# Kernel tuning notes

Hardware: AMD Instinct MI355X
Metric: run time of the kernel (lower is better)

The kernel has to match this reference:

```python
import jax, jax.numpy as jnp
import numpy as np

# Dims. NOTE: TransmorpherLayer2d passes (dim_head, num_heads) positionally into an
# attention class whose signature is (num_heads, dim_head) -> attention runs with
# H = dim_head = 64 heads of size Dh = num_heads = 12. embed_dim D = 768 either way.
B, S, L = 1, 64, 512
H, Dh = 64, 12
D = H * Dh          # 768
DFF = 3072
EPS = 1e-5


def _ln(x, g, b):
    m = x.mean(-1, keepdims=True)
    v = ((x - m) ** 2).mean(-1, keepdims=True)
    return (x - m) / jnp.sqrt(v + EPS) * g + b


def setup_inputs() -> dict:
    key = jax.random.key(0)
    ks = jax.random.split(key, 6)
    sd = 0.02
    p = {
        'x': jax.random.normal(ks[0], (B, S, L, D), jnp.float32),
        'w_row': jax.random.normal(ks[1], (D, 3 * D), jnp.float32) * sd,
        'b_row': jnp.zeros((3 * D,), jnp.float32),
        'w_col': jax.random.normal(ks[2], (D, 3 * D), jnp.float32) * sd,
        'b_col': jnp.zeros((3 * D,), jnp.float32),
        'g_a1': jnp.ones((D,), jnp.float32), 'be_a1': jnp.zeros((D,), jnp.float32),
        'g_a2': jnp.ones((D,), jnp.float32), 'be_a2': jnp.zeros((D,), jnp.float32),
        'w1': jax.random.normal(ks[3], (D, DFF), jnp.float32) * sd,
        'b1f': jnp.zeros((DFF,), jnp.float32),
        'w2': jax.random.normal(ks[4], (DFF, D), jnp.float32) * sd,
        'b2f': jnp.zeros((D,), jnp.float32),
        'g_n1': jnp.ones((D,), jnp.float32), 'be_n1': jnp.zeros((D,), jnp.float32),
        'g_n2': jnp.ones((D,), jnp.float32), 'be_n2': jnp.zeros((D,), jnp.float32),
    }
    return p


def reference(x, w_row, b_row, w_col, b_col, g_a1, be_a1, g_a2, be_a2,
              w1, b1f, w2, b2f, g_n1, be_n1, g_n2, be_n2):
    def qkv(t, w, b):
        q, k, v = jnp.split(t @ w + b, 3, axis=-1)
        rs = lambda a: a.reshape(B, S, L, H, Dh)
        return rs(q), rs(k), rs(v)

    # ---- TiedAxialSelfAttention2d (no 1/sqrt(d) scaling, tied over S) ----
    q, k, v = qkv(x, w_row, b_row)
    row_attn = jax.nn.softmax(jnp.einsum('bsihc,bsjhc->bhij', q, k), axis=-1)  # [B,H,L,L]
    row_out = jnp.einsum('bhij,bsjhd->bsihd', row_attn, v).reshape(B, S, L, D)
    out = _ln(x + row_out, g_a1, be_a1)

    q, k, v = qkv(out, w_col, b_col)
    col_attn = jax.nn.softmax(jnp.einsum('bilhc,bjlhc->bhijl', q, k), axis=-2)  # [B,H,S,S,L]
    col_out = jnp.einsum('bhijl,bjlhd->bilhd', col_attn, v).reshape(B, S, L, D)
    out = _ln(out + col_out, g_a2, be_a2)

    # ---- TransmorpherLayer2d residual + FFN (post-LN) ----
    y = _ln(x + out, g_n1, be_n1)
    ff = jax.nn.relu(y @ w1 + b1f) @ w2 + b2f
    return _ln(y + ff, g_n2, be_n2)
```

## Files before the change

kernel.cpp:

```cpp
#include <hip/hip_runtime.h>

typedef unsigned short u16;
typedef unsigned int u32;
typedef __attribute__((ext_vector_type(8))) short short8;
typedef __attribute__((ext_vector_type(4))) float floatx4;

#define LN_EPS 1e-5f
#define REG 6291456L

__device__ __forceinline__ float b2f(u16 u) {
    return __builtin_bit_cast(float, (u32)u << 16);
}
__device__ __forceinline__ u16 f2b(float f) {
    u32 x = __builtin_bit_cast(u32, f);
    return (u16)((x + 0x7fffu + ((x >> 16) & 1u)) >> 16);
}

__device__ __forceinline__ void ld12f(const float* p, float* d) {
    float4 a = ((const float4*)p)[0];
    float4 b = ((const float4*)p)[1];
    float4 c = ((const float4*)p)[2];
    d[0]=a.x; d[1]=a.y; d[2]=a.z;  d[3]=a.w;
    d[4]=b.x; d[5]=b.y; d[6]=b.z;  d[7]=b.w;
    d[8]=c.x; d[9]=c.y; d[10]=c.z; d[11]=c.w;
}
__device__ __forceinline__ void ld12b(const u16* p, float* d) {
    uint2 a = ((const uint2*)p)[0];
    uint2 b = ((const uint2*)p)[1];
    uint2 c = ((const uint2*)p)[2];
    d[0]=b2f((u16)a.x); d[1]=b2f((u16)(a.x>>16)); d[2]=b2f((u16)a.y);  d[3]=b2f((u16)(a.y>>16));
    d[4]=b2f((u16)b.x); d[5]=b2f((u16)(b.x>>16)); d[6]=b2f((u16)b.y);  d[7]=b2f((u16)(b.y>>16));
    d[8]=b2f((u16)c.x); d[9]=b2f((u16)(c.x>>16)); d[10]=b2f((u16)c.y); d[11]=b2f((u16)(c.y>>16));
}
__device__ __forceinline__ void st12f(float* p, const float* d) {
    ((float4*)p)[0] = make_float4(d[0], d[1], d[2], d[3]);
    ((float4*)p)[1] = make_float4(d[4], d[5], d[6], d[7]);
    ((float4*)p)[2] = make_float4(d[8], d[9], d[10], d[11]);
}
__device__ __forceinline__ void st12b(u16* p, const float* d) {
    uint2 a, b, c;
    a.x = (u32)f2b(d[0])  | ((u32)f2b(d[1])  << 16);
    a.y = (u32)f2b(d[2])  | ((u32)f2b(d[3])  << 16);
    b.x = (u32)f2b(d[4])  | ((u32)f2b(d[5])  << 16);
    b.y = (u32)f2b(d[6])  | ((u32)f2b(d[7])  << 16);
    c.x = (u32)f2b(d[8])  | ((u32)f2b(d[9])  << 16);
    c.y = (u32)f2b(d[10]) | ((u32)f2b(d[11]) << 16);
    ((uint2*)p)[0] = a; ((uint2*)p)[1] = b; ((uint2*)p)[2] = c;
}
__device__ __forceinline__ void wred2(float& a, float& b) {
#pragma unroll
    for (int o = 32; o > 0; o >>= 1) {
        a += __shfl_xor(a, o, 64);
        b += __shfl_xor(b, o, 64);
    }
}

__device__ __forceinline__ void gload16(const u16* g, u16* l) {
    __builtin_amdgcn_global_load_lds(
        (const __attribute__((address_space(1))) void*)g,
        (__attribute__((address_space(3))) void*)l, 16, 0, 0);
}

template<int N> __device__ __forceinline__ void wait_vm() {
    if constexpr (N == 0)      asm volatile("s_waitcnt vmcnt(0)" ::: "memory");
    else if constexpr (N == 4) asm volatile("s_waitcnt vmcnt(4)" ::: "memory");
    else if constexpr (N == 5) asm volatile("s_waitcnt vmcnt(5)" ::: "memory");
    else                       asm volatile("s_waitcnt vmcnt(0)" ::: "memory");
}

template<int BN_, int EPI, int RELU, int HASBIAS, int SMAJ>
__global__ __launch_bounds__(256, 2) void gemm_dma(
    const u16* __restrict__ A, const u16* __restrict__ BT,
    const float* __restrict__ bias, void* __restrict__ C,
    int Nb, int K, long sA, long sB, long sC, int colbase)
{
    constexpr int NCH  = (128 + BN_) / 64;
    constexpr int JF   = BN_ / 32;
    constexpr int TILE = (128 + BN_) * 32;
    __shared__ u16 lds[3 * TILE];

    const u16* Az = A + (long)blockIdx.z * sA;
    const u16* Bz = BT + (long)blockIdx.z * sB;
    const int n0 = blockIdx.x * BN_;
    const int tid = threadIdx.x;
    const int lane = tid & 63;
    const int wm = ((tid >> 6) >> 1) * 64;
    const int wn = ((tid >> 6) & 1) * (BN_ / 2);
    const int lrow = lane & 15;
    const int quad = lane >> 4;

    floatx4 acc[4][JF];
#pragma unroll
    for (int i = 0; i < 4; i++)
#pragma unroll
        for (int j = 0; j < JF; j++)
            acc[i][j] = (floatx4){0.f, 0.f, 0.f, 0.f};

    const u16* sbase[NCH];
    int doff[NCH];
#pragma unroll
    for (int it = 0; it < NCH; it++) {
        const int idx = tid + it * 256;
        const int slot = idx & 3;
        doff[it] = idx * 8;
        if (idx < 512) {
            const int row = idx >> 2;
            const int ch  = (slot ^ ((row >> 1) & 3)) * 8;
            const long grow = SMAJ
                ? ((long)(row >> 1) * 512 + (blockIdx.y << 1) + (row & 1))
                : ((long)blockIdx.y * 128 + row);
            sbase[it] = Az + grow * K + ch;
        } else {
            const int row = (idx - 512) >> 2;
            const int ch  = (slot ^ ((row >> 1) & 3)) * 8;
            sbase[it] = Bz + (long)(n0 + row) * K + ch;
        }
    }

    int aoff[4], boff[JF];
#pragma unroll
    for (int i = 0; i < 4; i++) {
        const int r = wm + i * 16 + lrow;
        aoff[i] = r * 32 + ((quad ^ ((r >> 1) & 3)) * 8);
    }
#pragma unroll
    for (int j = 0; j < JF; j++) {
        const int r = wn + j * 16 + lrow;
        boff[j] = 4096 + r * 32 + ((quad ^ ((r >> 1) & 3)) * 8);
    }

#pragma unroll
    for (int it = 0; it < NCH; it++)
        gload16(sbase[it], &lds[doff[it]]);
    if (K > 32) {
#pragma unroll
        for (int it = 0; it < NCH; it++)
            gload16(sbase[it] + 32, &lds[TILE + doff[it]]);
    }
    __builtin_amdgcn_sched_barrier(0);

    int bufc = 0;
    for (int kt = 0; kt < K; kt += 32) {
        if (kt + 32 >= K) wait_vm<0>();
        else              wait_vm<NCH>();
        __builtin_amdgcn_s_barrier();
        __builtin_amdgcn_sched_barrier(0);

        if (kt + 64 < K) {
            int nb = bufc + 2; if (nb >= 3) nb -= 3;
            const int nbo = nb * TILE;
#pragma unroll
            for (int it = 0; it < NCH; it++)
                gload16(sbase[it] + kt + 64, &lds[nbo + doff[it]]);
        }
        __builtin_amdgcn_sched_barrier(0);

        const int b0 = bufc * TILE;
        short8 af[4], bfr[JF];
#pragma unroll
        for (int i = 0; i < 4; i++)
            af[i] = *(const short8*)&lds[b0 + aoff[i]];
#pragma unroll
        for (int j = 0; j < JF; j++)
            bfr[j] = *(const short8*)&lds[b0 + boff[j]];
#pragma unroll
        for (int i = 0; i < 4; i++)
#pragma unroll
            for (int j = 0; j < JF; j++)
                acc[i][j] = __builtin_amdgcn_mfma_f32_16x16x32_bf16(
                    af[i], bfr[j], acc[i][j], 0, 0, 0);

        __builtin_amdgcn_sched_barrier(0);
        if (++bufc == 3) bufc = 0;
    }

    const int z = blockIdx.z;
#pragma unroll
    for (int j = 0; j < JF; j++) {
        const int n = n0 + wn + j * 16 + lrow;
        int t = 0, jj = n;
        if (EPI == 8 || EPI == 9) { t = n / 192; jj = n - t * 192; }
        const int hl = jj / 12;
        const int cc = jj - hl * 12;
        float bv = 0.f;
        if (HASBIAS)
            bv = (EPI == 8 || EPI == 9) ? bias[t * 768 + colbase + jj]
                                        : bias[colbase + n];
#pragma unroll
        for (int i = 0; i < 4; i++) {
            const int mb = wm + i * 16 + quad * 4;
#pragma unroll
            for (int r = 0; r < 4; r++) {
                const int ml = mb + r;
                float v = acc[i][j][r] + bv;
                if (RELU) v = fmaxf(v, 0.f);
                if (EPI == 0) {
                    const long m = (long)blockIdx.y * 128 + ml;
                    ((u16*)C)[m * Nb + n] = f2b(v);
                } else if (EPI == 1) {
                    const long m = (long)blockIdx.y * 128 + ml;
                    ((float*)C)[(long)z * sC + m * Nb + n] = v;
                } else if (EPI == 3) {
                    const int gm = blockIdx.y * 128 + ml;
                    const int s = gm >> 9, iL = gm & 511;
                    ((u16*)C)[(long)hl * 393216 + (long)(s * 12 + cc) * 512 + iL] = f2b(v);
                } else if (EPI == 4) {
                    const int m = blockIdx.y * 128 + ml;
                    ((u16*)C)[((long)hl * 512 + m) * 768 + colbase + z * 12 + cc] = f2b(v);
                } else if (EPI == 8) {
                    const int s = ml >> 1, iL = (blockIdx.y << 1) + (ml & 1);
                    ((u16*)C)[(long)t * REG + ((long)hl * 512 + iL) * 768 + s * 12 + cc] = f2b(v);
                } else if (EPI == 9) {
                    const int s = ml >> 1, l = (blockIdx.y << 1) + (ml & 1);
                    ((u16*)C)[(long)t * REG + (long)hl * 393216 + (long)l * 768 + s * 12 + cc] = f2b(v);
                }
            }
        }
    }
}

__global__ __launch_bounds__(256) void cast_kernel(
    const float* __restrict__ X, u16* __restrict__ Xb)
{
    const long i = ((long)blockIdx.x * 256 + threadIdx.x) * 8;
    float4 a = *(const float4*)(X + i);
    float4 b = *(const float4*)(X + i + 4);
    u16 t8[8] = { f2b(a.x), f2b(a.y), f2b(a.z), f2b(a.w),
                  f2b(b.x), f2b(b.y), f2b(b.z), f2b(b.w) };
    *(uint4*)(Xb + i) = *(const uint4*)t8;
}

__global__ __launch_bounds__(256) void transpose_kernel(
    const float* __restrict__ In, u16* __restrict__ Out, int R, int Ccols)
{
    __shared__ u16 tile[32][33];
    int tx = threadIdx.x & 31;
    int ty = threadIdx.x >> 5;
    int c0 = blockIdx.x * 32;
    int r0 = blockIdx.y * 32;
#pragma unroll
    for (int rr = 0; rr < 32; rr += 8)
        tile[ty + rr][tx] = f2b(In[(long)(r0 + ty + rr) * Ccols + c0 + tx]);
    __syncthreads();
#pragma unroll
    for (int rr = 0; rr < 32; rr += 8)
        Out[(long)(c0 + ty + rr) * R + r0 + tx] = tile[tx][ty + rr];
}

__global__ __launch_bounds__(256) void pack_qk_kernel(
    const float* __restrict__ In, u16* __restrict__ Out)
{
    __shared__ u16 tile[32][33];
    int tx = threadIdx.x & 31;
    int ty = threadIdx.x >> 5;
    int p0 = blockIdx.x * 32;
    int k0 = blockIdx.y * 32;
    int hg = p0 / 384, rem = p0 % 384;
    int t = rem / 192, j0 = rem % 192;
    int c0 = t * 768 + hg * 192 + j0;
#pragma unroll
    for (int rr = 0; rr < 32; rr += 8)
        tile[ty + rr][tx] = f2b(In[(long)(k0 + ty + rr) * 2304 + c0 + tx]);
    __syncthreads();
#pragma unroll
    for (int rr = 0; rr < 32; rr += 8)
        Out[(long)(p0 + ty + rr) * 768 + k0 + tx] = tile[tx][ty + rr];
}

__global__ __launch_bounds__(256) void pack_v_kernel(
    const float* __restrict__ In, u16* __restrict__ Out)
{
    __shared__ u16 tile[32][33];
    int tx = threadIdx.x & 31;
    int ty = threadIdx.x >> 5;
    int p0 = blockIdx.x * 32;
    int k0 = blockIdx.y * 32;
    int hg = p0 / 192, j0 = p0 % 192;
    int c0 = 1536 + hg * 192 + j0;
#pragma unroll
    for (int rr = 0; rr < 32; rr += 8)
        tile[ty + rr][tx] = f2b(In[(long)(k0 + ty + rr) * 2304 + c0 + tx]);
    __syncthreads();
#pragma unroll
    for (int rr = 0; rr < 32; rr += 8)
        Out[(long)(p0 + ty + rr) * 768 + k0 + tx] = tile[tx][ty + rr];
}

__global__ __launch_bounds__(256) void qkv_pack_kernel(
    const float* __restrict__ In, u16* __restrict__ Out)
{
    __shared__ u16 tile[32][33];
    int tx = threadIdx.x & 31;
    int ty = threadIdx.x >> 5;
    int p0 = blockIdx.x * 32;
    int k0 = blockIdx.y * 32;
    int hg = p0 / 576, r0 = p0 % 576;
    int t = r0 / 192, j0 = r0 % 192;
    int c0 = t * 768 + hg * 192 + j0;
#pragma unroll
    for (int rr = 0; rr < 32; rr += 8)
        tile[ty + rr][tx] = f2b(In[(long)(k0 + ty + rr) * 2304 + c0 + tx]);
    __syncthreads();
#pragma unroll
    for (int rr = 0; rr < 32; rr += 8)
        Out[(long)(p0 + ty + rr) * 768 + k0 + tx] = tile[tx][ty + rr];
}

__global__ __launch_bounds__(256) void softmax_kernel(
    const float* __restrict__ S, u16* __restrict__ P)
{
    const long r = (long)blockIdx.x * 4 + (threadIdx.x >> 6);
    const int lane = threadIdx.x & 63;
    const float* sp = S + r * 512 + lane * 8;
    float4 a = ((const float4*)sp)[0];
    float4 b = ((const float4*)sp)[1];
    float v[8] = {a.x, a.y, a.z, a.w, b.x, b.y, b.z, b.w};
    float mx = v[0];
#pragma unroll
    for (int e = 1; e < 8; e++) mx = fmaxf(mx, v[e]);
#pragma unroll
    for (int o = 32; o > 0; o >>= 1) mx = fmaxf(mx, __shfl_xor(mx, o, 64));
    float sum = 0.f;
#pragma unroll
    for (int e = 0; e < 8; e++) { v[e] = __expf(v[e] - mx); sum += v[e]; }
#pragma unroll
    for (int o = 32; o > 0; o >>= 1) sum += __shfl_xor(sum, o, 64);
    float inv = 1.0f / sum;
    uint4 o4;
    o4.x = (u32)f2b(v[0] * inv) | ((u32)f2b(v[1] * inv) << 16);
    o4.y = (u32)f2b(v[2] * inv) | ((u32)f2b(v[3] * inv) << 16);
    o4.z = (u32)f2b(v[4] * inv) | ((u32)f2b(v[5] * inv) << 16);
    o4.w = (u32)f2b(v[6] * inv) | ((u32)f2b(v[7] * inv) << 16);
    *(uint4*)(P + r * 512 + lane * 8) = o4;
}

template<int AF, int BF, int OF>
__global__ __launch_bounds__(256) void ln_add_kernel(
    const void* __restrict__ Xa, const void* __restrict__ Xb,
    const float* __restrict__ g, const float* __restrict__ be,
    void* __restrict__ Out)
{
    const long r = (long)blockIdx.x * 4 + (threadIdx.x >> 6);
    const int lane = threadIdx.x & 63;
    const long c0 = r * 768 + lane * 12;
    float va[12], vb[12], v[12];
    if (AF) ld12f((const float*)Xa + c0, va);
    else    ld12b((const u16*)Xa + c0, va);
    if (BF) ld12f((const float*)Xb + c0, vb);
    else    ld12b((const u16*)Xb + c0, vb);
    float sm = 0.f, s2 = 0.f;
#pragma unroll
    for (int e = 0; e < 12; e++) {
        v[e] = va[e] + vb[e];
        sm += v[e]; s2 += v[e] * v[e];
    }
    wred2(sm, s2);
    float mean = sm * (1.0f / 768.0f);
    float var  = s2 * (1.0f / 768.0f) - mean * mean;
    float rstd = rsqrtf(var + LN_EPS);
    float gv[12], bv[12], o[12];
    ld12f(g + lane * 12, gv);
    ld12f(be + lane * 12, bv);
#pragma unroll
    for (int e = 0; e < 12; e++)
        o[e] = (v[e] - mean) * rstd * gv[e] + bv[e];
    if (OF) st12f((float*)Out + c0, o);
    else    st12b((u16*)Out + c0, o);
}

__global__ __launch_bounds__(256) void ln_ln_kernel(
    const u16* __restrict__ A, const u16* __restrict__ B,
    const float* __restrict__ X,
    const float* __restrict__ g1, const float* __restrict__ be1,
    const float* __restrict__ g2, const float* __restrict__ be2,
    float* __restrict__ Out, u16* __restrict__ Outb)
{
    const long r = (long)blockIdx.x * 4 + (threadIdx.x >> 6);
    const int lane = threadIdx.x & 63;
    const long c0 = r * 768 + lane * 12;
    float ua[12], ub[12], u[12];
    ld12b(A + c0, ua);
    ld12b(B + c0, ub);
    float sm = 0.f, s2 = 0.f;
#pragma unroll
    for (int e = 0; e < 12; e++) {
        u[e] = ua[e] + ub[e];
        sm += u[e]; s2 += u[e] * u[e];
    }
    wred2(sm, s2);
    float mean1 = sm * (1.0f / 768.0f);
    float var1  = s2 * (1.0f / 768.0f) - mean1 * mean1;
    float rstd1 = rsqrtf(var1 + LN_EPS);

    float xx[12], g1v[12], b1v[12], w[12];
    ld12f(X + c0, xx);
    ld12f(g1 + lane * 12, g1v);
    ld12f(be1 + lane * 12, b1v);
    sm = 0.f; s2 = 0.f;
#pragma unroll
    for (int e = 0; e < 12; e++) {
        float tv = (u[e] - mean1) * rstd1 * g1v[e] + b1v[e];
        w[e] = xx[e] + tv;
        sm += w[e]; s2 += w[e] * w[e];
    }
    wred2(sm, s2);
    float mean2 = sm * (1.0f / 768.0f);
    float var2  = s2 * (1.0f / 768.0f) - mean2 * mean2;
    float rstd2 = rsqrtf(var2 + LN_EPS);

    float g2v[12], b2v[12], o[12];
    ld12f(g2 + lane * 12, g2v);
    ld12f(be2 + lane * 12, b2v);
#pragma unroll
    for (int e = 0; e < 12; e++)
        o[e] = (w[e] - mean2) * rstd2 * g2v[e] + b2v[e];
    st12f(Out + c0, o);
    st12b(Outb + c0, o);
}

__global__ __launch_bounds__(64) void col_attn_kernel(
    const u16* __restrict__ qc, const u16* __restrict__ kc,
    const u16* __restrict__ vc, u16* __restrict__ Out, int hbase)
{
    const int hh = blockIdx.x >> 9;
    const int l  = blockIdx.x & 511;
    const int i  = threadIdx.x;
    const long base = ((long)hh * 512 + l) * 768 + (long)i * 12;
    __shared__ float Ks[64][12];
    __shared__ float Vs[64][12];
    float q[12], kk[12], vv[12];
    ld12b(qc + base, q);
    ld12b(kc + base, kk);
    ld12b(vc + base, vv);
#pragma unroll
    for (int c = 0; c < 12; c++) { Ks[i][c] = kk[c]; Vs[i][c] = vv[c]; }
    __syncthreads();
    float sc[64];
#pragma unroll
    for (int j = 0; j < 64; j++) {
        float a = 0.f;
#pragma unroll
        for (int c = 0; c < 12; c++) a += q[c] * Ks[j][c];
        sc[j] = a;
    }
    float m = sc[0];
#pragma unroll
    for (int j = 1; j < 64; j++) m = fmaxf(m, sc[j]);
    float sum = 0.f;
#pragma unroll
    for (int j = 0; j < 64; j++) { sc[j] = __expf(sc[j] - m); sum += sc[j]; }
    float inv = 1.0f / sum;
    float o[12];
#pragma unroll
    for (int c = 0; c < 12; c++) o[c] = 0.f;
#pragma unroll
    for (int j = 0; j < 64; j++) {
        float p = sc[j] * inv;
#pragma unroll
        for (int c = 0; c < 12; c++) o[c] += p * Vs[j][c];
    }
    u16* op = Out + ((long)i * 512 + l) * 768 + hbase + hh * 12;
    st12b(op, o);
}

extern "C" void kernel_launch(void* const* d_in, const int* in_sizes, int n_in,
                              void* d_out, int out_size, void* d_ws, size_t ws_size,
                              hipStream_t stream)
{
    (void)in_sizes; (void)n_in; (void)out_size; (void)ws_size;

    const float* x     = (const float*)d_in[0];
    const float* w_row = (const float*)d_in[1];
    const float* b_row = (const float*)d_in[2];
    const float* w_col = (const float*)d_in[3];
    const float* b_col = (const float*)d_in[4];
    const float* g_a1  = (const float*)d_in[5];
    const float* be_a1 = (const float*)d_in[6];
    const float* g_a2  = (const float*)d_in[7];
    const float* be_a2 = (const float*)d_in[8];
    const float* w1    = (const float*)d_in[9];
    const float* b1f   = (const float*)d_in[10];
    const float* w2    = (const float*)d_in[11];
    const float* b2f_  = (const float*)d_in[12];
    const float* g_n1  = (const float*)d_in[13];
    const float* be_n1 = (const float*)d_in[14];
    const float* g_n2  = (const float*)d_in[15];
    const float* be_n2 = (const float*)d_in[16];
    float* outp = (float*)d_out;

    char* wp = (char*)d_ws;
    auto alloc = [&](size_t bytes) -> void* {
        void* p = (void*)wp;
        wp += (bytes + 255) & ~(size_t)255;
        return p;
    };
    u16*   wPqk   = (u16*)alloc((size_t)1536 * 768 * 2);
    u16*   wPv    = (u16*)alloc((size_t)768 * 768 * 2);
    u16*   wPcol  = (u16*)alloc((size_t)2304 * 768 * 2);
    u16*   w1T    = (u16*)alloc((size_t)3072 * 768 * 2);
    u16*   w2T    = (u16*)alloc((size_t)768 * 3072 * 2);
    u16*   bufA   = (u16*)alloc((size_t)32768 * 768 * 2);
    u16*   bufB   = (u16*)alloc((size_t)32768 * 768 * 2);
    u16*   qkvg   = (u16*)alloc((size_t)3 * 16 * 512 * 768 * 2);
    float* scores = (float*)alloc((size_t)16 * 512 * 512 * 4);
    u16*   probs  = (u16*)alloc((size_t)16 * 512 * 512 * 2);
    u16*   hidden = qkvg;
    u16*   xb     = bufB;
    u16*   ybf    = bufB;
    float* y      = outp;

    pack_qk_kernel<<<dim3(48, 24), 256, 0, stream>>>(w_row, wPqk);
    pack_v_kernel<<<dim3(24, 24), 256, 0, stream>>>(w_row, wPv);
    qkv_pack_kernel<<<dim3(72, 24), 256, 0, stream>>>(w_col, wPcol);
    transpose_kernel<<<dim3(96, 24), 256, 0, stream>>>(w1, w1T, 768, 3072);
    transpose_kernel<<<dim3(24, 96), 256, 0, stream>>>(w2, w2T, 3072, 768);
    cast_kernel<<<12288, 256, 0, stream>>>(x, xb);

    for (int hg = 0; hg < 4; hg++) {
        gemm_dma<192, 8, 0, 1, 1><<<dim3(2, 256), 256, 0, stream>>>(
            xb, wPqk + (long)hg * 384 * 768, b_row, qkvg,
            384, 768, 0, 0, 0, hg * 192);
        gemm_dma<192, 3, 0, 1, 0><<<dim3(1, 256), 256, 0, stream>>>(
            xb, wPv + (long)hg * 192 * 768, b_row, qkvg + 2 * REG,
            192, 768, 0, 0, 0, 1536 + hg * 192);
        gemm_dma<128, 1, 0, 0, 0><<<dim3(4, 4, 16), 256, 0, stream>>>(
            qkvg, qkvg + REG, nullptr, scores,
            512, 768, (long)512 * 768, (long)512 * 768, (long)512 * 512, 0);
        softmax_kernel<<<2048, 256, 0, stream>>>(scores, probs);
        gemm_dma<128, 4, 0, 0, 0><<<dim3(6, 4, 16), 256, 0, stream>>>(
            probs, qkvg + 2 * REG, nullptr, bufA,
            768, 512, (long)512 * 512, (long)768 * 512, 0, hg * 192);
    }
    ln_add_kernel<1, 0, 0><<<8192, 256, 0, stream>>>(x, bufA, g_a1, be_a1, bufB);

    for (int hg = 0; hg < 4; hg++) {
        gemm_dma<192, 9, 0, 1, 1><<<dim3(3, 256), 256, 0, stream>>>(
            bufB, wPcol + (long)hg * 576 * 768, b_col, qkvg,
            576, 768, 0, 0, 0, hg * 192);
        col_attn_kernel<<<8192, 64, 0, stream>>>(
            qkvg, qkvg + REG, qkvg + 2 * REG, bufA, hg * 192);
    }
    ln_ln_kernel<<<8192, 256, 0, stream>>>(
        bufB, bufA, x, g_a2, be_a2, g_n1, be_n1, y, ybf);

    for (int mc = 0; mc < 4; mc++) {
        const long off = (long)mc * 8192 * 768;
        gemm_dma<192, 0, 1, 1, 0><<<dim3(16, 64), 256, 0, stream>>>(
            ybf + off, w1T, b1f, hidden, 3072, 768, 0, 0, 0, 0);
        gemm_dma<192, 0, 0, 1, 0><<<dim3(4, 64), 256, 0, stream>>>(
            hidden, w2T, b2f_, bufA + off, 768, 3072, 0, 0, 0, 0);
    }
    ln_add_kernel<1, 0, 1><<<8192, 256, 0, stream>>>(y, bufA, g_n2, be_n2, outp);
}
```

Measured before the change: 1.580 ms.

## Process all attention heads in one pass when workspace allows, halve FFN chunks

When the workspace is large enough, the row and column attention stages run over all 64 heads in a single set of launches instead of four head-group loops. The QKV epilogues gain a head-group index and a runtime stride to support this, and probs reuses bufB. The FFN is split into two row chunks instead of four, using the larger hidden buffer. This cuts launch count and gives each launch a larger grid to fill the GPU, at the cost of a bigger workspace footprint and a fallback path that depends on ws_size.

Measured after the change: 1.431 ms. -9.4%, faster.

```diff
diff --git a/kernel.cpp b/kernel.cpp
--- a/kernel.cpp
+++ b/kernel.cpp
@@ -178,13 +178,14 @@
 #pragma unroll
     for (int j = 0; j < JF; j++) {
         const int n = n0 + wn + j * 16 + lrow;
-        int t = 0, jj = n;
-        if (EPI == 8 || EPI == 9) { t = n / 192; jj = n - t * 192; }
+        int t = 0, jj = n, hG = 0;
+        if (EPI == 8) { hG = n / 384; int rem = n - hG * 384; t = rem / 192; jj = rem - t * 192; }
+        if (EPI == 9) { hG = n / 576; int rem = n - hG * 576; t = rem / 192; jj = rem - t * 192; }
         const int hl = jj / 12;
         const int cc = jj - hl * 12;
         float bv = 0.f;
         if (HASBIAS)
-            bv = (EPI == 8 || EPI == 9) ? bias[t * 768 + colbase + jj]
+            bv = (EPI == 8 || EPI == 9) ? bias[t * 768 + colbase + hG * 192 + jj]
                                         : bias[colbase + n];
 #pragma unroll
         for (int i = 0; i < 4; i++) {
@@ -209,10 +210,10 @@
                     ((u16*)C)[((long)hl * 512 + m) * 768 + colbase + z * 12 + cc] = f2b(v);
                 } else if (EPI == 8) {
                     const int s = ml >> 1, iL = (blockIdx.y << 1) + (ml & 1);
-                    ((u16*)C)[(long)t * REG + ((long)hl * 512 + iL) * 768 + s * 12 + cc] = f2b(v);
+                    ((u16*)C)[(long)t * sC + ((long)(hG * 16 + hl) * 512 + iL) * 768 + s * 12 + cc] = f2b(v);
                 } else if (EPI == 9) {
                     const int s = ml >> 1, l = (blockIdx.y << 1) + (ml & 1);
-                    ((u16*)C)[(long)t * REG + (long)hl * 393216 + (long)l * 768 + s * 12 + cc] = f2b(v);
+                    ((u16*)C)[(long)t * sC + (long)(hG * 16 + hl) * 393216 + (long)l * 768 + s * 12 + cc] = f2b(v);
                 }
             }
         }
@@ -467,7 +468,7 @@
                               void* d_out, int out_size, void* d_ws, size_t ws_size,
                               hipStream_t stream)
 {
-    (void)in_sizes; (void)n_in; (void)out_size; (void)ws_size;
+    (void)in_sizes; (void)n_in; (void)out_size;
 
     const float* x     = (const float*)d_in[0];
     const float* w_row = (const float*)d_in[1];
@@ -501,9 +502,20 @@
     u16*   w2T    = (u16*)alloc((size_t)768 * 3072 * 2);
     u16*   bufA   = (u16*)alloc((size_t)32768 * 768 * 2);
     u16*   bufB   = (u16*)alloc((size_t)32768 * 768 * 2);
-    u16*   qkvg   = (u16*)alloc((size_t)3 * 16 * 512 * 768 * 2);
-    float* scores = (float*)alloc((size_t)16 * 512 * 512 * 4);
-    u16*   probs  = (u16*)alloc((size_t)16 * 512 * 512 * 2);
+
+    const size_t base_used   = (size_t)(wp - (char*)d_ws);
+    const size_t need_merged = base_used
+        + (size_t)3 * 64 * 393216 * 2
+        + (size_t)64 * 512 * 512 * 4 + 512;
+    const bool merged = (ws_size >= need_merged);
+    const int  NH = merged ? 64 : 16;
+    const int  NG = merged ? 1 : 4;
+    const long QS = (long)NH * 393216;
+
+    u16*   qkvg   = (u16*)alloc((size_t)3 * NH * 393216 * 2);
+    float* scores = (float*)alloc((size_t)NH * 512 * 512 * 4);
+    u16*   probs  = merged ? bufB
+                           : (u16*)alloc((size_t)16 * 512 * 512 * 2);
     u16*   hidden = qkvg;
     u16*   xb     = bufB;
     u16*   ybf    = bufB;
@@ -516,38 +528,40 @@
     transpose_kernel<<<dim3(24, 96), 256, 0, stream>>>(w2, w2T, 3072, 768);
     cast_kernel<<<12288, 256, 0, stream>>>(x, xb);
 
-    for (int hg = 0; hg < 4; hg++) {
-        gemm_dma<192, 8, 0, 1, 1><<<dim3(2, 256), 256, 0, stream>>>(
-            xb, wPqk + (long)hg * 384 * 768, b_row, qkvg,
-            384, 768, 0, 0, 0, hg * 192);
-        gemm_dma<192, 3, 0, 1, 0><<<dim3(1, 256), 256, 0, stream>>>(
-            xb, wPv + (long)hg * 192 * 768, b_row, qkvg + 2 * REG,
-            192, 768, 0, 0, 0, 1536 + hg * 192);
-        gemm_dma<128, 1, 0, 0, 0><<<dim3(4, 4, 16), 256, 0, stream>>>(
-            qkvg, qkvg + REG, nullptr, scores,
+    for (int g = 0; g < NG; g++) {
+        gemm_dma<192, 8, 0, 1, 1><<<dim3(NH / 8, 256), 256, 0, stream>>>(
+            xb, wPqk + (long)g * 384 * 768, b_row, qkvg,
+            24 * NH, 768, 0, 0, QS, g * 192);
+        gemm_dma<192, 3, 0, 1, 0><<<dim3(NH / 16, 256), 256, 0, stream>>>(
+            xb, wPv + (long)g * 192 * 768, b_row, qkvg + 2 * QS,
+            12 * NH, 768, 0, 0, 0, 1536 + g * 192);
+        gemm_dma<128, 1, 0, 0, 0><<<dim3(4, 4, NH), 256, 0, stream>>>(
+            qkvg, qkvg + QS, nullptr, scores,
             512, 768, (long)512 * 768, (long)512 * 768, (long)512 * 512, 0);
-        softmax_kernel<<<2048, 256, 0, stream>>>(scores, probs);
-        gemm_dma<128, 4, 0, 0, 0><<<dim3(6, 4, 16), 256, 0, stream>>>(
-            probs, qkvg + 2 * REG, nullptr, bufA,
-            768, 512, (long)512 * 512, (long)768 * 512, 0, hg * 192);
+        softmax_kernel<<<NH * 128, 256, 0, stream>>>(scores, probs);
+        gemm_dma<128, 4, 0, 0, 0><<<dim3(6, 4, NH), 256, 0, stream>>>(
+            probs, qkvg + 2 * QS, nullptr, bufA,
+            768, 512, (long)512 * 512, (long)768 * 512, 0, g * 192);
     }
     ln_add_kernel<1, 0, 0><<<8192, 256, 0, stream>>>(x, bufA, g_a1, be_a1, bufB);
 
-    for (int hg = 0; hg < 4; hg++) {
-        gemm_dma<192, 9, 0, 1, 1><<<dim3(3, 256), 256, 0, stream>>>(
-            bufB, wPcol + (long)hg * 576 * 768, b_col, qkvg,
-            576, 768, 0, 0, 0, hg * 192);
-        col_attn_kernel<<<8192, 64, 0, stream>>>(
-            qkvg, qkvg + REG, qkvg + 2 * REG, bufA, hg * 192);
+    for (int g = 0; g < NG; g++) {
+        gemm_dma<192, 9, 0, 1, 1><<<dim3(3 * NH / 16, 256), 256, 0, stream>>>(
+            bufB, wPcol + (long)g * 576 * 768, b_col, qkvg,
+            36 * NH, 768, 0, 0, QS, g * 192);
+        col_attn_kernel<<<NH * 512, 64, 0, stream>>>(
+            qkvg, qkvg + QS, qkvg + 2 * QS, bufA, g * 192);
     }
     ln_ln_kernel<<<8192, 256, 0, stream>>>(
         bufB, bufA, x, g_a2, be_a2, g_n1, be_n1, y, ybf);
 
-    for (int mc = 0; mc < 4; mc++) {
-        const long off = (long)mc * 8192 * 768;
-        gemm_dma<192, 0, 1, 1, 0><<<dim3(16, 64), 256, 0, stream>>>(
+    const int nchunk = merged ? 2 : 4;
+    const int crows  = 32768 / nchunk;
+    for (int mc = 0; mc < nchunk; mc++) {
+        const long off = (long)mc * crows * 768;
+        gemm_dma<192, 0, 1, 1, 0><<<dim3(16, crows / 128), 256, 0, stream>>>(
             ybf + off, w1T, b1f, hidden, 3072, 768, 0, 0, 0, 0);
-        gemm_dma<192, 0, 0, 1, 0><<<dim3(4, 64), 256, 0, stream>>>(
+        gemm_dma<192, 0, 0, 1, 0><<<dim3(4, crows / 128), 256, 0, stream>>>(
             hidden, w2T, b2f_, bufA + off, 768, 3072, 0, 0, 0, 0);
     }
     ln_add_kernel<1, 0, 1><<<8192, 256, 0, stream>>>(y, bufA, g_n2, be_n2, outp);
```
